# Kernel tuning notes

Hardware: AMD Instinct MI355X
Metric: run time of the kernel (lower is better)

The kernel has to match this reference:

```python
import jax, jax.numpy as jnp
import numpy as np

B, D, R = 8192, 4096, 64
REG_W, REG_C = 0.01, 0.05


def setup_inputs() -> dict:
    key = jax.random.key(0)
    ks = jax.random.split(key, 7)
    return {
        "X": jax.random.normal(ks[0], (B, D), dtype=jnp.float32),
        "U1": jax.random.normal(ks[1], (1, D, R), dtype=jnp.float32),
        "U2": jax.random.normal(ks[2], (2, D, R), dtype=jnp.float32),
        "U3": jax.random.normal(ks[3], (3, D, R), dtype=jnp.float32),
        "C": jax.random.normal(ks[4], (3,), dtype=jnp.float32),
        "beta": jax.random.normal(ks[5], (1,), dtype=jnp.float32),
        "C_sin": jax.random.normal(ks[6], (1,), dtype=jnp.float32),
    }


def reference(X, U1, U2, U3, C, beta, C_sin):
    # term_j(x) = sum_r prod_{i<=j} <x, U_j[i, :, r]>
    result = jnp.broadcast_to(beta[0], (X.shape[0],))
    reg_loss_w = jnp.float32(0.0)
    for j, U in enumerate((U1, U2, U3)):
        dots = jnp.einsum("bd,odr->obr", X, U)      # [order, B, R]
        term = jnp.prod(dots, axis=0).sum(axis=1)   # [B]
        result = result + C[j] * term
        reg_loss_w = reg_loss_w + REG_W * (jnp.abs(U).sum() / U.size)
    sine_term = C_sin[0] * jnp.sin(X).sum(axis=1)
    result = result + sine_term
    reg_loss_c = REG_C * (jnp.abs(C).sum() + jnp.abs(C_sin).sum())
    total_reg = reg_loss_w + reg_loss_c
    return result, total_reg
```

## Files before the change

### kernel.cpp

```cpp
#include <hip/hip_runtime.h>
#include <hip/hip_bf16.h>

typedef float f32x4 __attribute__((ext_vector_type(4)));
typedef short s16x8 __attribute__((ext_vector_type(8)));

#define D_DIM 4096
#define NT 24
#define BM 128
#define NBODY 32
#define BOFF 0
#define AOFF 24576
#define SINW_OFF 3145728u
#define PART_OFF 3276800u

__device__ __forceinline__ unsigned short f2bf(float f) {
    unsigned u = __float_as_uint(f);
    u += 0x7fffu + ((u >> 16) & 1u);
    return (unsigned short)(u >> 16);
}

__device__ __forceinline__ void gload16(const void* g, void* l) {
    __builtin_amdgcn_global_load_lds(
        (const __attribute__((address_space(1))) unsigned int*)g,
        (__attribute__((address_space(3))) unsigned int*)l, 16, 0, 0);
}

__global__ __launch_bounds__(64) void reg_init_kernel(const float* __restrict__ C,
                                                      const float* __restrict__ Csin,
                                                      float* __restrict__ reg_out) {
    if (threadIdx.x == 0)
        reg_out[0] = 0.05f * (fabsf(C[0]) + fabsf(C[1]) + fabsf(C[2]) + fabsf(Csin[0]));
}

__global__ __launch_bounds__(64) void build_w_kernel(const float* __restrict__ U1,
                                                     const float* __restrict__ U2,
                                                     const float* __restrict__ U3,
                                                     unsigned short* __restrict__ W,
                                                     float* __restrict__ reg_out) {
    const int ks = blockIdx.x / NT;
    const int ct = blockIdx.x % NT;
    const int l  = threadIdx.x;
    const int n  = ct * 16 + (l & 15);
    const int kb = ks * 32 + ((l >> 4) << 3);

    const float* src;
    float scale;
    if (n < 64)       { src = U1 + n;                  scale = 0.01f / 262144.f; }
    else if (n < 128) { src = U2 + (n - 64);           scale = 0.01f / 524288.f; }
    else if (n < 192) { src = U2 + 262144 + (n - 128); scale = 0.01f / 524288.f; }
    else if (n < 256) { src = U3 + (n - 192);          scale = 0.01f / 786432.f; }
    else if (n < 320) { src = U3 + 262144 + (n - 256); scale = 0.01f / 786432.f; }
    else              { src = U3 + 524288 + (n - 320); scale = 0.01f / 786432.f; }

    unsigned short h[8];
    float sabs = 0.f;
#pragma unroll
    for (int j = 0; j < 8; ++j) {
        float u = src[(size_t)(kb + j) * 64];
        sabs += fabsf(u);
        h[j] = f2bf(u);
    }
    uint4 pk;
    pk.x = (unsigned)h[0] | ((unsigned)h[1] << 16);
    pk.y = (unsigned)h[2] | ((unsigned)h[3] << 16);
    pk.z = (unsigned)h[4] | ((unsigned)h[5] << 16);
    pk.w = (unsigned)h[6] | ((unsigned)h[7] << 16);
    *(uint4*)(W + ((size_t)blockIdx.x * 64 + l) * 8) = pk;

    sabs *= scale;
#pragma unroll
    for (int off = 32; off >= 1; off >>= 1)
        sabs += __shfl_xor(sabs, off, 64);
    if (l == 0) atomicAdd(reg_out, sabs);
}

__global__ __launch_bounds__(512, 4) void poly_main_kernel(const float* __restrict__ X,
                                                           const unsigned short* __restrict__ W,
                                                           _Float16* __restrict__ part,
                                                           float* __restrict__ sinws) {
    __shared__ __align__(16) char pool[40960];

    const int t    = threadIdx.x;
    const int lane = t & 63;
    const int wv   = t >> 6;
    const int rg   = wv >> 2;
    const int cg   = wv & 3;
    const int ct0  = cg * 3;
    const int rb   = blockIdx.x >> 3;
    const int cs   = (blockIdx.x >> 2) & 1;
    const int kh   = blockIdx.x & 3;
    const int row0 = rb * BM;
    const bool doSin = (cs == 0);

    const int sr = t >> 2;
    const int q  = t & 3;
    const float* xp = X + (size_t)(row0 + sr) * D_DIM + kh * 1024 + q * 8;
    const int awfrag = (sr >> 4) * 1024 + (((q << 4) | (sr & 15)) << 4);

    const int nB  = (wv < 4) ? 2 : 1;
    const int ch0 = (wv < 4) ? (wv * 2) : (4 + wv);
    const int slab0 = kh * 32;
    const unsigned short* wbase = W + (size_t)slab0 * 12288 + cs * 6144
                                    + ch0 * 512 + lane * 8;

    f32x4 acc[4][3];
#pragma unroll
    for (int r = 0; r < 4; ++r)
#pragma unroll
        for (int c = 0; c < 3; ++c) acc[r][c] = (f32x4){0.f, 0.f, 0.f, 0.f};
    float sinacc = 0.f;
    f32x4 xn0, xn1;

#define STAGE(bufl, XA, XB)                                                     \
    {                                                                           \
        if (doSin)                                                              \
            sinacc += __sinf(XA.x) + __sinf(XA.y) + __sinf(XA.z) + __sinf(XA.w) \
                    + __sinf(XB.x) + __sinf(XB.y) + __sinf(XB.z) + __sinf(XB.w);\
        uint4 h_;                                                               \
        h_.x = (unsigned)f2bf(XA.x) | ((unsigned)f2bf(XA.y) << 16);             \
        h_.y = (unsigned)f2bf(XA.z) | ((unsigned)f2bf(XA.w) << 16);             \
        h_.z = (unsigned)f2bf(XB.x) | ((unsigned)f2bf(XB.y) << 16);             \
        h_.w = (unsigned)f2bf(XB.z) | ((unsigned)f2bf(XB.w) << 16);             \
        *(uint4*)(pool + AOFF + (bufl) * 8192 + awfrag) = h_;                   \
    }

    gload16(wbase, pool + BOFF + ch0 * 1024);
    if (nB == 2) gload16(wbase + 512, pool + BOFF + (ch0 + 1) * 1024);
    {
        f32x4 x00 = *(const f32x4*)xp;
        f32x4 x01 = *(const f32x4*)(xp + 4);
        STAGE(0, x00, x01);
        xn0 = *(const f32x4*)(xp + 32);
        xn1 = *(const f32x4*)(xp + 36);
    }
    asm volatile("s_waitcnt lgkmcnt(0)" ::: "memory");
    asm volatile("s_waitcnt vmcnt(2)" ::: "memory");
    __builtin_amdgcn_s_barrier();
    __builtin_amdgcn_sched_barrier(0);

#define BODY(d_, CUR, NXT)                                                      \
    {                                                                           \
        const int d__ = (d_);                                                   \
        if (d__ + 1 < NBODY) {                                                  \
            const unsigned short* g_ = wbase + (size_t)(d__ + 1) * 12288;       \
            gload16(g_, pool + BOFF + (NXT) * 12288 + ch0 * 1024);              \
            if (nB == 2)                                                        \
                gload16(g_ + 512, pool + BOFF + (NXT) * 12288 + (ch0 + 1) * 1024);\
        }                                                                       \
        int sl_ = d__ + 2; if (sl_ > NBODY - 1) sl_ = NBODY - 1;                \
        f32x4 xf0_ = *(const f32x4*)(xp + (size_t)sl_ * 32);                    \
        f32x4 xf1_ = *(const f32x4*)(xp + (size_t)sl_ * 32 + 4);                \
        if (d__ + 1 < NBODY) { STAGE(NXT, xn0, xn1); }                          \
        xn0 = xf0_; xn1 = xf1_;                                                 \
        const char* ab_ = pool + AOFF + (CUR) * 8192;                           \
        const char* bb_ = pool + BOFF + (CUR) * 12288;                          \
        s16x8 af0_ = *(const s16x8*)(ab_ + (rg * 4 + 0) * 1024 + lane * 16);    \
        s16x8 af1_ = *(const s16x8*)(ab_ + (rg * 4 + 1) * 1024 + lane * 16);    \
        s16x8 af2_ = *(const s16x8*)(ab_ + (rg * 4 + 2) * 1024 + lane * 16);    \
        s16x8 af3_ = *(const s16x8*)(ab_ + (rg * 4 + 3) * 1024 + lane * 16);    \
        s16x8 bf0_ = *(const s16x8*)(bb_ + (ct0 + 0) * 1024 + lane * 16);       \
        s16x8 bf1_ = *(const s16x8*)(bb_ + (ct0 + 1) * 1024 + lane * 16);       \
        s16x8 bf2_ = *(const s16x8*)(bb_ + (ct0 + 2) * 1024 + lane * 16);       \
        asm volatile("s_waitcnt lgkmcnt(0)" ::: "memory");                      \
        __builtin_amdgcn_sched_barrier(0);                                      \
        __builtin_amdgcn_s_setprio(1);                                          \
        acc[0][0] = __builtin_amdgcn_mfma_f32_16x16x32_bf16(af0_, bf0_, acc[0][0], 0, 0, 0); \
        acc[0][1] = __builtin_amdgcn_mfma_f32_16x16x32_bf16(af0_, bf1_, acc[0][1], 0, 0, 0); \
        acc[0][2] = __builtin_amdgcn_mfma_f32_16x16x32_bf16(af0_, bf2_, acc[0][2], 0, 0, 0); \
        acc[1][0] = __builtin_amdgcn_mfma_f32_16x16x32_bf16(af1_, bf0_, acc[1][0], 0, 0, 0); \
        acc[1][1] = __builtin_amdgcn_mfma_f32_16x16x32_bf16(af1_, bf1_, acc[1][1], 0, 0, 0); \
        acc[1][2] = __builtin_amdgcn_mfma_f32_16x16x32_bf16(af1_, bf2_, acc[1][2], 0, 0, 0); \
        acc[2][0] = __builtin_amdgcn_mfma_f32_16x16x32_bf16(af2_, bf0_, acc[2][0], 0, 0, 0); \
        acc[2][1] = __builtin_amdgcn_mfma_f32_16x16x32_bf16(af2_, bf1_, acc[2][1], 0, 0, 0); \
        acc[2][2] = __builtin_amdgcn_mfma_f32_16x16x32_bf16(af2_, bf2_, acc[2][2], 0, 0, 0); \
        acc[3][0] = __builtin_amdgcn_mfma_f32_16x16x32_bf16(af3_, bf0_, acc[3][0], 0, 0, 0); \
        acc[3][1] = __builtin_amdgcn_mfma_f32_16x16x32_bf16(af3_, bf1_, acc[3][1], 0, 0, 0); \
        acc[3][2] = __builtin_amdgcn_mfma_f32_16x16x32_bf16(af3_, bf2_, acc[3][2], 0, 0, 0); \
        __builtin_amdgcn_s_setprio(0);                                          \
        asm volatile("s_waitcnt vmcnt(2)" ::: "memory");                        \
        __builtin_amdgcn_s_barrier();                                           \
        __builtin_amdgcn_sched_barrier(0);                                      \
    }

    for (int d = 0; d < NBODY; d += 2) {
        BODY(d, 0, 1);
        BODY(d + 1, 1, 0);
    }
#undef BODY
#undef STAGE

    _Float16* pb = part + (size_t)kh * 8192 * 384;
    const int lr4 = (lane >> 4) << 2;
    const int lc  = lane & 15;
#pragma unroll
    for (int rf = 0; rf < 4; ++rf)
#pragma unroll
        for (int c = 0; c < 3; ++c) {
            const int col = cs * 192 + (ct0 + c) * 16 + lc;
#pragma unroll
            for (int i = 0; i < 4; ++i) {
                const int rl = rg * 64 + rf * 16 + lr4 + i;
                pb[(size_t)(row0 + rl) * 384 + col] = (_Float16)acc[rf][c][i];
            }
        }

    if (doSin) {
        sinacc += __shfl_xor(sinacc, 1);
        sinacc += __shfl_xor(sinacc, 2);
        if ((t & 3) == 0)
            sinws[(size_t)kh * 8192 + row0 + sr] = sinacc;
    }
}

__global__ __launch_bounds__(512) void combine_kernel(const _Float16* __restrict__ part,
                                                      const float* __restrict__ sinws,
                                                      const float* __restrict__ C,
                                                      const float* __restrict__ beta,
                                                      const float* __restrict__ Csin,
                                                      float* __restrict__ out) {
    const int t   = threadIdx.x;
    const int row = blockIdx.x * 32 + (t >> 4);
    const int cc  = t & 15;
    const size_t rbase = (size_t)row * 384;

    float t1 = 0.f, t2 = 0.f, t3 = 0.f;
#pragma unroll
    for (int j = 0; j < 4; ++j) {
        const int c = j * 16 + cc;
        float a1 = 0.f, a2 = 0.f, b2 = 0.f, a3 = 0.f, b3 = 0.f, c3 = 0.f;
#pragma unroll
        for (int qq = 0; qq < 4; ++qq) {
            const _Float16* p = part + (size_t)qq * 8192 * 384 + rbase;
            a1 += (float)p[c];
            a2 += (float)p[64 + c];
            b2 += (float)p[128 + c];
            a3 += (float)p[192 + c];
            b3 += (float)p[256 + c];
            c3 += (float)p[320 + c];
        }
        t1 += a1;
        t2 += a2 * b2;
        t3 += a3 * b3 * c3;
    }
#pragma unroll
    for (int off = 1; off < 16; off <<= 1) {
        t1 += __shfl_xor(t1, off, 16);
        t2 += __shfl_xor(t2, off, 16);
        t3 += __shfl_xor(t3, off, 16);
    }
    if (cc == 0) {
        const float s = sinws[row] + sinws[8192 + row]
                      + sinws[2 * 8192 + row] + sinws[3 * 8192 + row];
        out[row] = beta[0] + C[0] * t1 + C[1] * t2 + C[2] * t3 + Csin[0] * s;
    }
}

extern "C" void kernel_launch(void* const* d_in, const int* in_sizes, int n_in,
                              void* d_out, int out_size, void* d_ws, size_t ws_size,
                              hipStream_t stream) {
    const float* X   = (const float*)d_in[0];
    const float* U1  = (const float*)d_in[1];
    const float* U2  = (const float*)d_in[2];
    const float* U3  = (const float*)d_in[3];
    const float* Cc  = (const float*)d_in[4];
    const float* bet = (const float*)d_in[5];
    const float* Cs  = (const float*)d_in[6];
    float* out = (float*)d_out;

    unsigned short* W = (unsigned short*)d_ws;
    float* sinws = (float*)((char*)d_ws + SINW_OFF);
    _Float16* part = (_Float16*)((char*)d_ws + PART_OFF);

    reg_init_kernel<<<1, 64, 0, stream>>>(Cc, Cs, out + 8192);
    build_w_kernel<<<128 * NT, 64, 0, stream>>>(U1, U2, U3, W, out + 8192);
    poly_main_kernel<<<512, 512, 0, stream>>>(X, W, part, sinws);
    combine_kernel<<<256, 512, 0, stream>>>(part, sinws, Cc, bet, Cs, out);
}
```

Before: 102.1 us.

## Split X bf16 packing and sin into separate kernel, pure-DMA triple-buffered GEMM

Moves X conversion to bf16 and the sin row-sum into a standalone pack kernel writing MFMA-fragment-ordered bf16 X to workspace. The GEMM kernel then loads both operands via global_load_lds with a three-stage buffer, a 128x96 tile and split-K across two halves and two launches. This removes VALU conversion and transcendental work from the MFMA loop, but adds a global round trip for packed X and doubles the partial-sum slices the combine step must read.

```diff
diff --git a/kernel.cpp b/kernel.cpp
--- a/kernel.cpp
+++ b/kernel.cpp
@@ -6,12 +6,9 @@
 
 #define D_DIM 4096
 #define NT 24
-#define BM 128
-#define NBODY 32
-#define BOFF 0
-#define AOFF 24576
 #define SINW_OFF 3145728u
-#define PART_OFF 3276800u
+#define PART_OFF 3407872u
+#define XBF_OFF  28573696u
 
 __device__ __forceinline__ unsigned short f2bf(float f) {
     unsigned u = __float_as_uint(f);
@@ -74,142 +71,144 @@
     if (l == 0) atomicAdd(reg_out, sabs);
 }
 
-__global__ __launch_bounds__(512, 4) void poly_main_kernel(const float* __restrict__ X,
-                                                           const unsigned short* __restrict__ W,
-                                                           _Float16* __restrict__ part,
-                                                           float* __restrict__ sinws) {
-    __shared__ __align__(16) char pool[40960];
+__global__ __launch_bounds__(512) void pack_kernel(const float* __restrict__ X,
+                                                   unsigned short* __restrict__ Xbf,
+                                                   float* __restrict__ sinws,
+                                                   int kh) {
+    const int t    = threadIdx.x;
+    const int rb   = blockIdx.x >> 2;
+    const int ks   = blockIdx.x & 3;
+    const int row  = t >> 2;
+    const int q    = t & 3;
+    const int row0 = rb * 128;
+
+    const float* xp = X + (size_t)(row0 + row) * D_DIM + kh * 2048 + ks * 512 + q * 8;
+    const int lane_o = (q << 4) | (row & 15);
+    const int rf     = row >> 4;
+
+    float sinacc = 0.f;
+#pragma unroll 4
+    for (int s = 0; s < 16; ++s) {
+        f32x4 a = *(const f32x4*)(xp + s * 32);
+        f32x4 b = *(const f32x4*)(xp + s * 32 + 4);
+        sinacc += __sinf(a.x) + __sinf(a.y) + __sinf(a.z) + __sinf(a.w)
+                + __sinf(b.x) + __sinf(b.y) + __sinf(b.z) + __sinf(b.w);
+        uint4 pk;
+        pk.x = (unsigned)f2bf(a.x) | ((unsigned)f2bf(a.y) << 16);
+        pk.y = (unsigned)f2bf(a.z) | ((unsigned)f2bf(a.w) << 16);
+        pk.z = (unsigned)f2bf(b.x) | ((unsigned)f2bf(b.y) << 16);
+        pk.w = (unsigned)f2bf(b.z) | ((unsigned)f2bf(b.w) << 16);
+        const size_t chunk = (size_t)(rb * 64 + ks * 16 + s) * 8 + rf;
+        *(uint4*)(Xbf + chunk * 512 + lane_o * 8) = pk;
+    }
+    sinacc += __shfl_xor(sinacc, 1);
+    sinacc += __shfl_xor(sinacc, 2);
+    if (q == 0)
+        sinws[(size_t)(kh * 4 + ks) * 8192 + row0 + row] = sinacc;
+}
+
+__global__ __launch_bounds__(512, 4) void gemm_kernel(const unsigned short* __restrict__ Xbf,
+                                                      const unsigned short* __restrict__ W,
+                                                      _Float16* __restrict__ part,
+                                                      int kh) {
+    __shared__ __align__(16) char pool[43008];
+    const int BOFF2 = 24576;
 
     const int t    = threadIdx.x;
     const int lane = t & 63;
     const int wv   = t >> 6;
-    const int rg   = wv >> 2;
-    const int cg   = wv & 3;
-    const int ct0  = cg * 3;
-    const int rb   = blockIdx.x >> 3;
-    const int cs   = (blockIdx.x >> 2) & 1;
-    const int kh   = blockIdx.x & 3;
-    const int row0 = rb * BM;
-    const bool doSin = (cs == 0);
-
-    const int sr = t >> 2;
-    const int q  = t & 3;
-    const float* xp = X + (size_t)(row0 + sr) * D_DIM + kh * 1024 + q * 8;
-    const int awfrag = (sr >> 4) * 1024 + (((q << 4) | (sr & 15)) << 4);
-
-    const int nB  = (wv < 4) ? 2 : 1;
-    const int ch0 = (wv < 4) ? (wv * 2) : (4 + wv);
-    const int slab0 = kh * 32;
-    const unsigned short* wbase = W + (size_t)slab0 * 12288 + cs * 6144
-                                    + ch0 * 512 + lane * 8;
-
-    f32x4 acc[4][3];
-#pragma unroll
-    for (int r = 0; r < 4; ++r)
+    const int rg   = wv >> 1;
+    const int cg   = wv & 1;
+    const int bid  = blockIdx.x;
+    const int rb   = bid >> 3;
+    const int cs   = (bid >> 1) & 3;
+    const int kq   = bid & 1;
+    const int row0 = rb * 128;
+    const int khk  = kh * 64 + kq * 32;
+    const int kqb  = kq * 32;
+
+#define ISSUE(dd_, bufi_)                                                       \
+    {                                                                           \
+        int dc_ = (dd_) > 31 ? 31 : (dd_);                                      \
+        if (wv < 4) {                                                           \
+            const unsigned short* ga_ = Xbf                                     \
+                + ((size_t)((rb * 64 + kqb + dc_) * 8 + 2 * wv)) * 512          \
+                + lane * 8;                                                     \
+            gload16(ga_, pool + (bufi_) * 8192 + 2 * wv * 1024);                \
+            gload16(ga_ + 512, pool + (bufi_) * 8192 + (2 * wv + 1) * 1024);    \
+        } else {                                                                \
+            const int c0_ = (wv == 4) ? 0 : (wv == 5) ? 2 : (wv == 6) ? 4 : 5;  \
+            const unsigned short* gb_ = W                                       \
+                + ((size_t)(khk + dc_) * 24 + cs * 6 + c0_) * 512 + lane * 8;   \
+            gload16(gb_, pool + BOFF2 + (bufi_) * 6144 + c0_ * 1024);           \
+            if (wv < 6)                                                         \
+                gload16(gb_ + 512, pool + BOFF2 + (bufi_) * 6144 + (c0_ + 1) * 1024); \
+        }                                                                       \
+    }
+
+    f32x4 acc[2][3];
+#pragma unroll
+    for (int r = 0; r < 2; ++r)
 #pragma unroll
         for (int c = 0; c < 3; ++c) acc[r][c] = (f32x4){0.f, 0.f, 0.f, 0.f};
-    float sinacc = 0.f;
-    f32x4 xn0, xn1;
-
-#define STAGE(bufl, XA, XB)                                                     \
-    {                                                                           \
-        if (doSin)                                                              \
-            sinacc += __sinf(XA.x) + __sinf(XA.y) + __sinf(XA.z) + __sinf(XA.w) \
-                    + __sinf(XB.x) + __sinf(XB.y) + __sinf(XB.z) + __sinf(XB.w);\
-        uint4 h_;                                                               \
-        h_.x = (unsigned)f2bf(XA.x) | ((unsigned)f2bf(XA.y) << 16);             \
-        h_.y = (unsigned)f2bf(XA.z) | ((unsigned)f2bf(XA.w) << 16);             \
-        h_.z = (unsigned)f2bf(XB.x) | ((unsigned)f2bf(XB.y) << 16);             \
-        h_.w = (unsigned)f2bf(XB.z) | ((unsigned)f2bf(XB.w) << 16);             \
-        *(uint4*)(pool + AOFF + (bufl) * 8192 + awfrag) = h_;                   \
-    }
-
-    gload16(wbase, pool + BOFF + ch0 * 1024);
-    if (nB == 2) gload16(wbase + 512, pool + BOFF + (ch0 + 1) * 1024);
-    {
-        f32x4 x00 = *(const f32x4*)xp;
-        f32x4 x01 = *(const f32x4*)(xp + 4);
-        STAGE(0, x00, x01);
-        xn0 = *(const f32x4*)(xp + 32);
-        xn1 = *(const f32x4*)(xp + 36);
-    }
-    asm volatile("s_waitcnt lgkmcnt(0)" ::: "memory");
-    asm volatile("s_waitcnt vmcnt(2)" ::: "memory");
+
+    ISSUE(0, 0);
+    ISSUE(1, 1);
+    if (wv < 6) { asm volatile("s_waitcnt vmcnt(2)" ::: "memory"); }
+    else        { asm volatile("s_waitcnt vmcnt(1)" ::: "memory"); }
     __builtin_amdgcn_s_barrier();
     __builtin_amdgcn_sched_barrier(0);
 
-#define BODY(d_, CUR, NXT)                                                      \
+#define BODY(d_, CUR, ISS)                                                      \
     {                                                                           \
-        const int d__ = (d_);                                                   \
-        if (d__ + 1 < NBODY) {                                                  \
-            const unsigned short* g_ = wbase + (size_t)(d__ + 1) * 12288;       \
-            gload16(g_, pool + BOFF + (NXT) * 12288 + ch0 * 1024);              \
-            if (nB == 2)                                                        \
-                gload16(g_ + 512, pool + BOFF + (NXT) * 12288 + (ch0 + 1) * 1024);\
-        }                                                                       \
-        int sl_ = d__ + 2; if (sl_ > NBODY - 1) sl_ = NBODY - 1;                \
-        f32x4 xf0_ = *(const f32x4*)(xp + (size_t)sl_ * 32);                    \
-        f32x4 xf1_ = *(const f32x4*)(xp + (size_t)sl_ * 32 + 4);                \
-        if (d__ + 1 < NBODY) { STAGE(NXT, xn0, xn1); }                          \
-        xn0 = xf0_; xn1 = xf1_;                                                 \
-        const char* ab_ = pool + AOFF + (CUR) * 8192;                           \
-        const char* bb_ = pool + BOFF + (CUR) * 12288;                          \
-        s16x8 af0_ = *(const s16x8*)(ab_ + (rg * 4 + 0) * 1024 + lane * 16);    \
-        s16x8 af1_ = *(const s16x8*)(ab_ + (rg * 4 + 1) * 1024 + lane * 16);    \
-        s16x8 af2_ = *(const s16x8*)(ab_ + (rg * 4 + 2) * 1024 + lane * 16);    \
-        s16x8 af3_ = *(const s16x8*)(ab_ + (rg * 4 + 3) * 1024 + lane * 16);    \
-        s16x8 bf0_ = *(const s16x8*)(bb_ + (ct0 + 0) * 1024 + lane * 16);       \
-        s16x8 bf1_ = *(const s16x8*)(bb_ + (ct0 + 1) * 1024 + lane * 16);       \
-        s16x8 bf2_ = *(const s16x8*)(bb_ + (ct0 + 2) * 1024 + lane * 16);       \
+        ISSUE((d_) + 2, ISS);                                                   \
+        const char* ab_ = pool + (CUR) * 8192 + rg * 2048;                      \
+        const char* bb_ = pool + BOFF2 + (CUR) * 6144 + cg * 3072;              \
+        s16x8 a0_ = *(const s16x8*)(ab_ + lane * 16);                           \
+        s16x8 a1_ = *(const s16x8*)(ab_ + 1024 + lane * 16);                    \
+        s16x8 b0_ = *(const s16x8*)(bb_ + lane * 16);                           \
+        s16x8 b1_ = *(const s16x8*)(bb_ + 1024 + lane * 16);                    \
+        s16x8 b2_ = *(const s16x8*)(bb_ + 2048 + lane * 16);                    \
         asm volatile("s_waitcnt lgkmcnt(0)" ::: "memory");                      \
         __builtin_amdgcn_sched_barrier(0);                                      \
         __builtin_amdgcn_s_setprio(1);                                          \
-        acc[0][0] = __builtin_amdgcn_mfma_f32_16x16x32_bf16(af0_, bf0_, acc[0][0], 0, 0, 0); \
-        acc[0][1] = __builtin_amdgcn_mfma_f32_16x16x32_bf16(af0_, bf1_, acc[0][1], 0, 0, 0); \
-        acc[0][2] = __builtin_amdgcn_mfma_f32_16x16x32_bf16(af0_, bf2_, acc[0][2], 0, 0, 0); \
-        acc[1][0] = __builtin_amdgcn_mfma_f32_16x16x32_bf16(af1_, bf0_, acc[1][0], 0, 0, 0); \
-        acc[1][1] = __builtin_amdgcn_mfma_f32_16x16x32_bf16(af1_, bf1_, acc[1][1], 0, 0, 0); \
-        acc[1][2] = __builtin_amdgcn_mfma_f32_16x16x32_bf16(af1_, bf2_, acc[1][2], 0, 0, 0); \
-        acc[2][0] = __builtin_amdgcn_mfma_f32_16x16x32_bf16(af2_, bf0_, acc[2][0], 0, 0, 0); \
-        acc[2][1] = __builtin_amdgcn_mfma_f32_16x16x32_bf16(af2_, bf1_, acc[2][1], 0, 0, 0); \
-        acc[2][2] = __builtin_amdgcn_mfma_f32_16x16x32_bf16(af2_, bf2_, acc[2][2], 0, 0, 0); \
-        acc[3][0] = __builtin_amdgcn_mfma_f32_16x16x32_bf16(af3_, bf0_, acc[3][0], 0, 0, 0); \
-        acc[3][1] = __builtin_amdgcn_mfma_f32_16x16x32_bf16(af3_, bf1_, acc[3][1], 0, 0, 0); \
-        acc[3][2] = __builtin_amdgcn_mfma_f32_16x16x32_bf16(af3_, bf2_, acc[3][2], 0, 0, 0); \
+        acc[0][0] = __builtin_amdgcn_mfma_f32_16x16x32_bf16(a0_, b0_, acc[0][0], 0, 0, 0); \
+        acc[0][1] = __builtin_amdgcn_mfma_f32_16x16x32_bf16(a0_, b1_, acc[0][1], 0, 0, 0); \
+        acc[0][2] = __builtin_amdgcn_mfma_f32_16x16x32_bf16(a0_, b2_, acc[0][2], 0, 0, 0); \
+        acc[1][0] = __builtin_amdgcn_mfma_f32_16x16x32_bf16(a1_, b0_, acc[1][0], 0, 0, 0); \
+        acc[1][1] = __builtin_amdgcn_mfma_f32_16x16x32_bf16(a1_, b1_, acc[1][1], 0, 0, 0); \
+        acc[1][2] = __builtin_amdgcn_mfma_f32_16x16x32_bf16(a1_, b2_, acc[1][2], 0, 0, 0); \
         __builtin_amdgcn_s_setprio(0);                                          \
-        asm volatile("s_waitcnt vmcnt(2)" ::: "memory");                        \
+        if (wv < 6) { asm volatile("s_waitcnt vmcnt(2)" ::: "memory"); }        \
+        else        { asm volatile("s_waitcnt vmcnt(1)" ::: "memory"); }        \
         __builtin_amdgcn_s_barrier();                                           \
         __builtin_amdgcn_sched_barrier(0);                                      \
     }
 
-    for (int d = 0; d < NBODY; d += 2) {
-        BODY(d, 0, 1);
+    for (int d = 0; d < 30; d += 3) {
+        BODY(d,     0, 2);
         BODY(d + 1, 1, 0);
-    }
+        BODY(d + 2, 2, 1);
+    }
+    BODY(30, 0, 2);
+    BODY(31, 1, 0);
 #undef BODY
-#undef STAGE
-
-    _Float16* pb = part + (size_t)kh * 8192 * 384;
+#undef ISSUE
+
+    _Float16* pb = part + (size_t)(kh * 2 + kq) * 8192 * 384;
     const int lr4 = (lane >> 4) << 2;
     const int lc  = lane & 15;
 #pragma unroll
-    for (int rf = 0; rf < 4; ++rf)
+    for (int rf = 0; rf < 2; ++rf)
 #pragma unroll
         for (int c = 0; c < 3; ++c) {
-            const int col = cs * 192 + (ct0 + c) * 16 + lc;
+            const int col = cs * 96 + (cg * 3 + c) * 16 + lc;
 #pragma unroll
             for (int i = 0; i < 4; ++i) {
-                const int rl = rg * 64 + rf * 16 + lr4 + i;
+                const int rl = rg * 32 + rf * 16 + lr4 + i;
                 pb[(size_t)(row0 + rl) * 384 + col] = (_Float16)acc[rf][c][i];
             }
         }
-
-    if (doSin) {
-        sinacc += __shfl_xor(sinacc, 1);
-        sinacc += __shfl_xor(sinacc, 2);
-        if ((t & 3) == 0)
-            sinws[(size_t)kh * 8192 + row0 + sr] = sinacc;
-    }
 }
 
 __global__ __launch_bounds__(512) void combine_kernel(const _Float16* __restrict__ part,
@@ -249,8 +248,10 @@
         t3 += __shfl_xor(t3, off, 16);
     }
     if (cc == 0) {
-        const float s = sinws[row] + sinws[8192 + row]
-                      + sinws[2 * 8192 + row] + sinws[3 * 8192 + row];
+        float s = 0.f;
+#pragma unroll
+        for (int v = 0; v < 8; ++v)
+            s += sinws[(size_t)v * 8192 + row];
         out[row] = beta[0] + C[0] * t1 + C[1] * t2 + C[2] * t3 + Csin[0] * s;
     }
 }
@@ -267,12 +268,16 @@
     const float* Cs  = (const float*)d_in[6];
     float* out = (float*)d_out;
 
-    unsigned short* W = (unsigned short*)d_ws;
-    float* sinws = (float*)((char*)d_ws + SINW_OFF);
-    _Float16* part = (_Float16*)((char*)d_ws + PART_OFF);
+    unsigned short* W   = (unsigned short*)d_ws;
+    float* sinws        = (float*)((char*)d_ws + SINW_OFF);
+    _Float16* part      = (_Float16*)((char*)d_ws + PART_OFF);
+    unsigned short* Xbf = (unsigned short*)((char*)d_ws + XBF_OFF);
 
     reg_init_kernel<<<1, 64, 0, stream>>>(Cc, Cs, out + 8192);
     build_w_kernel<<<128 * NT, 64, 0, stream>>>(U1, U2, U3, W, out + 8192);
-    poly_main_kernel<<<512, 512, 0, stream>>>(X, W, part, sinws);
+    pack_kernel<<<256, 512, 0, stream>>>(X, Xbf, sinws, 0);
+    gemm_kernel<<<512, 512, 0, stream>>>(Xbf, W, part, 0);
+    pack_kernel<<<256, 512, 0, stream>>>(X, Xbf, sinws, 1);
+    gemm_kernel<<<512, 512, 0, stream>>>(Xbf, W, part, 1);
     combine_kernel<<<256, 512, 0, stream>>>(part, sinws, Cc, bet, Cs, out);
 }
```

Measured after the change: 144.4 us. 1.41x slower.

## Replace software-pipelined main GEMM loop with simple synchronous 64-row tiles

Applied to the files above, without the earlier changes.

The main kernel drops the double-buffered, prefetching pipeline with explicit waitcnt and priority control. It moves to 64-row blocks of 256 threads that load two K-slabs per iteration and synchronise with plain __syncthreads before and after the MFMAs. Grid size doubles to 1024 blocks and each wave now covers all rows with 3 column tiles. The aim is higher occupancy and simpler code. The cost is that global-to-LDS load latency is no longer overlapped with compute, and the W tiles get reloaded by twice as many blocks.

```diff
diff --git a/kernel.cpp b/kernel.cpp
--- a/kernel.cpp
+++ b/kernel.cpp
@@ -6,9 +6,8 @@
 
 #define D_DIM 4096
 #define NT 24
-#define BM 128
-#define NBODY 32
-#define BOFF 0
+#define BM 64
+#define NBODY 16
 #define AOFF 24576
 #define SINW_OFF 3145728u
 #define PART_OFF 3276800u
@@ -74,34 +73,27 @@
     if (l == 0) atomicAdd(reg_out, sabs);
 }
 
-__global__ __launch_bounds__(512, 4) void poly_main_kernel(const float* __restrict__ X,
+__global__ __launch_bounds__(256, 3) void poly_main_kernel(const float* __restrict__ X,
                                                            const unsigned short* __restrict__ W,
                                                            _Float16* __restrict__ part,
                                                            float* __restrict__ sinws) {
-    __shared__ __align__(16) char pool[40960];
+    __shared__ __align__(16) char pool[32768];
 
     const int t    = threadIdx.x;
     const int lane = t & 63;
     const int wv   = t >> 6;
-    const int rg   = wv >> 2;
-    const int cg   = wv & 3;
-    const int ct0  = cg * 3;
-    const int rb   = blockIdx.x >> 3;
-    const int cs   = (blockIdx.x >> 2) & 1;
-    const int kh   = blockIdx.x & 3;
+    const int bid  = blockIdx.x;
+    const int rb   = bid >> 3;
+    const int cs   = (bid >> 2) & 1;
+    const int ks   = bid & 3;
     const int row0 = rb * BM;
     const bool doSin = (cs == 0);
 
     const int sr = t >> 2;
     const int q  = t & 3;
-    const float* xp = X + (size_t)(row0 + sr) * D_DIM + kh * 1024 + q * 8;
-    const int awfrag = (sr >> 4) * 1024 + (((q << 4) | (sr & 15)) << 4);
-
-    const int nB  = (wv < 4) ? 2 : 1;
-    const int ch0 = (wv < 4) ? (wv * 2) : (4 + wv);
-    const int slab0 = kh * 32;
-    const unsigned short* wbase = W + (size_t)slab0 * 12288 + cs * 6144
-                                    + ch0 * 512 + lane * 8;
+    const float* xp = X + (size_t)(row0 + sr) * D_DIM + ks * 1024 + q * 8;
+    const int aw0 = AOFF + (sr >> 4) * 1024 + (((q << 4) | (sr & 15)) << 4);
+    const int aw1 = aw0 + 4096;
 
     f32x4 acc[4][3];
 #pragma unroll
@@ -109,106 +101,67 @@
 #pragma unroll
         for (int c = 0; c < 3; ++c) acc[r][c] = (f32x4){0.f, 0.f, 0.f, 0.f};
     float sinacc = 0.f;
-    f32x4 xn0, xn1;
-
-#define STAGE(bufl, XA, XB)                                                     \
-    {                                                                           \
-        if (doSin)                                                              \
-            sinacc += __sinf(XA.x) + __sinf(XA.y) + __sinf(XA.z) + __sinf(XA.w) \
-                    + __sinf(XB.x) + __sinf(XB.y) + __sinf(XB.z) + __sinf(XB.w);\
-        uint4 h_;                                                               \
-        h_.x = (unsigned)f2bf(XA.x) | ((unsigned)f2bf(XA.y) << 16);             \
-        h_.y = (unsigned)f2bf(XA.z) | ((unsigned)f2bf(XA.w) << 16);             \
-        h_.z = (unsigned)f2bf(XB.x) | ((unsigned)f2bf(XB.y) << 16);             \
-        h_.w = (unsigned)f2bf(XB.z) | ((unsigned)f2bf(XB.w) << 16);             \
-        *(uint4*)(pool + AOFF + (bufl) * 8192 + awfrag) = h_;                   \
-    }
-
-    gload16(wbase, pool + BOFF + ch0 * 1024);
-    if (nB == 2) gload16(wbase + 512, pool + BOFF + (ch0 + 1) * 1024);
-    {
-        f32x4 x00 = *(const f32x4*)xp;
-        f32x4 x01 = *(const f32x4*)(xp + 4);
-        STAGE(0, x00, x01);
-        xn0 = *(const f32x4*)(xp + 32);
-        xn1 = *(const f32x4*)(xp + 36);
-    }
-    asm volatile("s_waitcnt lgkmcnt(0)" ::: "memory");
-    asm volatile("s_waitcnt vmcnt(2)" ::: "memory");
-    __builtin_amdgcn_s_barrier();
-    __builtin_amdgcn_sched_barrier(0);
-
-#define BODY(d_, CUR, NXT)                                                      \
-    {                                                                           \
-        const int d__ = (d_);                                                   \
-        if (d__ + 1 < NBODY) {                                                  \
-            const unsigned short* g_ = wbase + (size_t)(d__ + 1) * 12288;       \
-            gload16(g_, pool + BOFF + (NXT) * 12288 + ch0 * 1024);              \
-            if (nB == 2)                                                        \
-                gload16(g_ + 512, pool + BOFF + (NXT) * 12288 + (ch0 + 1) * 1024);\
-        }                                                                       \
-        int sl_ = d__ + 2; if (sl_ > NBODY - 1) sl_ = NBODY - 1;                \
-        f32x4 xf0_ = *(const f32x4*)(xp + (size_t)sl_ * 32);                    \
-        f32x4 xf1_ = *(const f32x4*)(xp + (size_t)sl_ * 32 + 4);                \
-        if (d__ + 1 < NBODY) { STAGE(NXT, xn0, xn1); }                          \
-        xn0 = xf0_; xn1 = xf1_;                                                 \
-        const char* ab_ = pool + AOFF + (CUR) * 8192;                           \
-        const char* bb_ = pool + BOFF + (CUR) * 12288;                          \
-        s16x8 af0_ = *(const s16x8*)(ab_ + (rg * 4 + 0) * 1024 + lane * 16);    \
-        s16x8 af1_ = *(const s16x8*)(ab_ + (rg * 4 + 1) * 1024 + lane * 16);    \
-        s16x8 af2_ = *(const s16x8*)(ab_ + (rg * 4 + 2) * 1024 + lane * 16);    \
-        s16x8 af3_ = *(const s16x8*)(ab_ + (rg * 4 + 3) * 1024 + lane * 16);    \
-        s16x8 bf0_ = *(const s16x8*)(bb_ + (ct0 + 0) * 1024 + lane * 16);       \
-        s16x8 bf1_ = *(const s16x8*)(bb_ + (ct0 + 1) * 1024 + lane * 16);       \
-        s16x8 bf2_ = *(const s16x8*)(bb_ + (ct0 + 2) * 1024 + lane * 16);       \
-        asm volatile("s_waitcnt lgkmcnt(0)" ::: "memory");                      \
-        __builtin_amdgcn_sched_barrier(0);                                      \
-        __builtin_amdgcn_s_setprio(1);                                          \
-        acc[0][0] = __builtin_amdgcn_mfma_f32_16x16x32_bf16(af0_, bf0_, acc[0][0], 0, 0, 0); \
-        acc[0][1] = __builtin_amdgcn_mfma_f32_16x16x32_bf16(af0_, bf1_, acc[0][1], 0, 0, 0); \
-        acc[0][2] = __builtin_amdgcn_mfma_f32_16x16x32_bf16(af0_, bf2_, acc[0][2], 0, 0, 0); \
-        acc[1][0] = __builtin_amdgcn_mfma_f32_16x16x32_bf16(af1_, bf0_, acc[1][0], 0, 0, 0); \
-        acc[1][1] = __builtin_amdgcn_mfma_f32_16x16x32_bf16(af1_, bf1_, acc[1][1], 0, 0, 0); \
-        acc[1][2] = __builtin_amdgcn_mfma_f32_16x16x32_bf16(af1_, bf2_, acc[1][2], 0, 0, 0); \
-        acc[2][0] = __builtin_amdgcn_mfma_f32_16x16x32_bf16(af2_, bf0_, acc[2][0], 0, 0, 0); \
-        acc[2][1] = __builtin_amdgcn_mfma_f32_16x16x32_bf16(af2_, bf1_, acc[2][1], 0, 0, 0); \
-        acc[2][2] = __builtin_amdgcn_mfma_f32_16x16x32_bf16(af2_, bf2_, acc[2][2], 0, 0, 0); \
-        acc[3][0] = __builtin_amdgcn_mfma_f32_16x16x32_bf16(af3_, bf0_, acc[3][0], 0, 0, 0); \
-        acc[3][1] = __builtin_amdgcn_mfma_f32_16x16x32_bf16(af3_, bf1_, acc[3][1], 0, 0, 0); \
-        acc[3][2] = __builtin_amdgcn_mfma_f32_16x16x32_bf16(af3_, bf2_, acc[3][2], 0, 0, 0); \
-        __builtin_amdgcn_s_setprio(0);                                          \
-        asm volatile("s_waitcnt vmcnt(2)" ::: "memory");                        \
-        __builtin_amdgcn_s_barrier();                                           \
-        __builtin_amdgcn_sched_barrier(0);                                      \
-    }
-
-    for (int d = 0; d < NBODY; d += 2) {
-        BODY(d, 0, 1);
-        BODY(d + 1, 1, 0);
-    }
-#undef BODY
-#undef STAGE
-
-    _Float16* pb = part + (size_t)kh * 8192 * 384;
+
+    for (int d = 0; d < NBODY; ++d) {
+        const size_t slabg = (size_t)(ks * 32 + 2 * d);
+#pragma unroll
+        for (int ksl = 0; ksl < 2; ++ksl)
+#pragma unroll
+            for (int j = 0; j < 3; ++j) {
+                const unsigned short* g = W
+                    + ((slabg + ksl) * 24 + cs * 12 + wv * 3 + j) * 512 + lane * 8;
+                gload16(g, pool + ksl * 12288 + (wv * 3 + j) * 1024);
+            }
+#pragma unroll
+        for (int ksl = 0; ksl < 2; ++ksl) {
+            f32x4 a = *(const f32x4*)(xp + d * 64 + ksl * 32);
+            f32x4 b = *(const f32x4*)(xp + d * 64 + ksl * 32 + 4);
+            if (doSin)
+                sinacc += __sinf(a.x) + __sinf(a.y) + __sinf(a.z) + __sinf(a.w)
+                        + __sinf(b.x) + __sinf(b.y) + __sinf(b.z) + __sinf(b.w);
+            uint4 pk;
+            pk.x = (unsigned)f2bf(a.x) | ((unsigned)f2bf(a.y) << 16);
+            pk.y = (unsigned)f2bf(a.z) | ((unsigned)f2bf(a.w) << 16);
+            pk.z = (unsigned)f2bf(b.x) | ((unsigned)f2bf(b.y) << 16);
+            pk.w = (unsigned)f2bf(b.z) | ((unsigned)f2bf(b.w) << 16);
+            *(uint4*)(pool + (ksl ? aw1 : aw0)) = pk;
+        }
+        __syncthreads();
+
+#pragma unroll
+        for (int ksl = 0; ksl < 2; ++ksl) {
+            s16x8 b0 = *(const s16x8*)(pool + ksl * 12288 + (wv * 3 + 0) * 1024 + lane * 16);
+            s16x8 b1 = *(const s16x8*)(pool + ksl * 12288 + (wv * 3 + 1) * 1024 + lane * 16);
+            s16x8 b2 = *(const s16x8*)(pool + ksl * 12288 + (wv * 3 + 2) * 1024 + lane * 16);
+#pragma unroll
+            for (int rf = 0; rf < 4; ++rf) {
+                s16x8 af = *(const s16x8*)(pool + AOFF + (ksl * 4 + rf) * 1024 + lane * 16);
+                acc[rf][0] = __builtin_amdgcn_mfma_f32_16x16x32_bf16(af, b0, acc[rf][0], 0, 0, 0);
+                acc[rf][1] = __builtin_amdgcn_mfma_f32_16x16x32_bf16(af, b1, acc[rf][1], 0, 0, 0);
+                acc[rf][2] = __builtin_amdgcn_mfma_f32_16x16x32_bf16(af, b2, acc[rf][2], 0, 0, 0);
+            }
+        }
+        __syncthreads();
+    }
+
+    _Float16* pb = part + (size_t)ks * 8192 * 384;
     const int lr4 = (lane >> 4) << 2;
     const int lc  = lane & 15;
 #pragma unroll
     for (int rf = 0; rf < 4; ++rf)
 #pragma unroll
         for (int c = 0; c < 3; ++c) {
-            const int col = cs * 192 + (ct0 + c) * 16 + lc;
-#pragma unroll
-            for (int i = 0; i < 4; ++i) {
-                const int rl = rg * 64 + rf * 16 + lr4 + i;
-                pb[(size_t)(row0 + rl) * 384 + col] = (_Float16)acc[rf][c][i];
-            }
+            const int col = cs * 192 + (wv * 3 + c) * 16 + lc;
+#pragma unroll
+            for (int i = 0; i < 4; ++i)
+                pb[(size_t)(row0 + rf * 16 + lr4 + i) * 384 + col] = (_Float16)acc[rf][c][i];
         }
 
     if (doSin) {
         sinacc += __shfl_xor(sinacc, 1);
         sinacc += __shfl_xor(sinacc, 2);
-        if ((t & 3) == 0)
-            sinws[(size_t)kh * 8192 + row0 + sr] = sinacc;
+        if (q == 0)
+            sinws[(size_t)ks * 8192 + row0 + sr] = sinacc;
     }
 }
 
@@ -273,6 +226,6 @@
 
     reg_init_kernel<<<1, 64, 0, stream>>>(Cc, Cs, out + 8192);
     build_w_kernel<<<128 * NT, 64, 0, stream>>>(U1, U2, U3, W, out + 8192);
-    poly_main_kernel<<<512, 512, 0, stream>>>(X, W, part, sinws);
+    poly_main_kernel<<<1024, 256, 0, stream>>>(X, W, part, sinws);
     combine_kernel<<<256, 512, 0, stream>>>(part, sinws, Cc, bet, Cs, out);
 }
```

Measured after the change: 105.1 us. 1.03x slower.
